# Performance work log

Hardware: AMD Instinct MI355X
Metric: run time of the kernel (lower is better)

## Reference

```python
import jax, jax.numpy as jnp
import numpy as np

P = 16                     # patch size
D = 192                    # embed dim (forced by SAT d_model=192)
NHEAD = 3                  # ViT-Tiny heads
SAT_H, SAT_DK, SAT_DV = 8, 32, 32
N_SLICE = 10
PER_LI = jnp.linspace(0.1, 1.0, N_SLICE)
LN_EPS = 1e-5


def layernorm(z, g, b):
    m = z.mean(-1, keepdims=True)
    v = ((z - m) ** 2).mean(-1, keepdims=True)
    return (z - m) * jax.lax.rsqrt(v + LN_EPS) * g + b


def setup_inputs() -> dict:
    key = jax.random.key(0)
    ks = jax.random.split(key, 32)
    B, IMG, DEPTH, MLP = 128, 224, 12, 4 * D
    S = (IMG // P) ** 2 + 1  # 197 tokens
    n = lambda k, sh: jax.random.normal(k, sh, jnp.float32) * 0.02
    z = lambda sh: jnp.zeros(sh, jnp.float32)
    o = lambda sh: jnp.ones(sh, jnp.float32)
    return {
        "x": jax.random.uniform(ks[0], (B, 3, IMG, IMG), jnp.float32),
        "x_g_norm": jax.random.uniform(ks[1], (B, 1, 56, 56), jnp.float32),
        "patch_w": n(ks[2], (D, 3, P, P)), "patch_b": z((D,)),
        "cls_token": n(ks[3], (1, 1, D)), "pos_embed": n(ks[4], (1, S, D)),
        "eleva_embed": n(ks[5], (1, D)),
        "sat_wq": n(ks[6], (D, SAT_H * SAT_DK)), "sat_bq": z((SAT_H * SAT_DK,)),
        "sat_wk": n(ks[7], (D, SAT_H * SAT_DK)), "sat_bk": z((SAT_H * SAT_DK,)),
        "sat_wv": n(ks[8], (D, SAT_H * SAT_DV)), "sat_bv": z((SAT_H * SAT_DV,)),
        "sat_wo": n(ks[9], (SAT_H * SAT_DV, D)), "sat_bo": z((D,)),
        "ln1_g": o((DEPTH, D)), "ln1_b": z((DEPTH, D)),
        "qkv_w": n(ks[10], (DEPTH, D, 3 * D)), "qkv_b": z((DEPTH, 3 * D)),
        "proj_w": n(ks[11], (DEPTH, D, D)), "proj_b": z((DEPTH, D)),
        "ln2_g": o((DEPTH, D)), "ln2_b": z((DEPTH, D)),
        "fc1_w": n(ks[12], (DEPTH, D, MLP)), "fc1_b": z((DEPTH, MLP)),
        "fc2_w": n(ks[13], (DEPTH, MLP, D)), "fc2_b": z((DEPTH, D)),
        "norm_g": o((D,)), "norm_b": z((D,)),
    }


def _forward(x, x_g_norm, patch_w, patch_b, cls_token, pos_embed, eleva_embed,
             sat_wq, sat_bq, sat_wk, sat_bk, sat_wv, sat_bv, sat_wo, sat_bo,
             ln1_g, ln1_b, qkv_w, qkv_b, proj_w, proj_b, ln2_g, ln2_b,
             fc1_w, fc1_b, fc2_w, fc2_b, norm_g, norm_b):
    B = x.shape[0]
    # --- patch embed: Conv2d(3, D, kernel=P, stride=P) -> [B, N, D] ---
    feat = jax.lax.conv_general_dilated(
        x, patch_w, (P, P), 'VALID', dimension_numbers=('NCHW', 'OIHW', 'NCHW'))
    feat = feat + patch_b[None, :, None, None]
    tokens = feat.reshape(B, D, -1).transpose(0, 2, 1)          # [B, 196, D]
    tok = jnp.concatenate([jnp.broadcast_to(cls_token, (B, 1, D)), tokens], axis=1)
    tok = tok + pos_embed                                        # [B, S, D]
    S = tok.shape[1]
    # --- elevation weight per sample (vectorized bisect + linear interp) ---
    means = x_g_norm.mean(axis=(1, 2, 3))                        # [B]
    idx = jnp.clip(jnp.searchsorted(PER_LI, means, side='left'), 0, N_SLICE - 1)
    per_hi = PER_LI[idx]
    per_lo = jnp.where(idx == 0, 0.0, PER_LI[jnp.maximum(idx - 1, 0)])
    idx_f = idx.astype(jnp.float32)
    idx_inter = idx_f - (per_hi - means) / (per_hi - per_lo)
    w = jnp.where(idx == N_SLICE - 1, idx_f, idx_inter) / N_SLICE  # [B]
    # --- SAT fusion: per (batch, token) a 2-element attention over (token, ele) ---
    ele = jnp.broadcast_to(eleva_embed[0] * w[:, None, None], tok.shape)  # [B,S,D]
    at_in = jnp.stack([tok, ele], axis=2)                        # [B, S, 2, D]
    q = (at_in @ sat_wq + sat_bq).reshape(B, S, 2, SAT_H, SAT_DK)
    k = (at_in @ sat_wk + sat_bk).reshape(B, S, 2, SAT_H, SAT_DK)
    v = (at_in @ sat_wv + sat_bv).reshape(B, S, 2, SAT_H, SAT_DV)
    att = jnp.einsum('bsqhd,bskhd->bshqk', q, k) * (1.0 / np.sqrt(SAT_DK))
    att = jax.nn.softmax(att, axis=-1)
    sat_o = jnp.einsum('bshqk,bskhd->bsqhd', att, v).reshape(B, S, 2, SAT_H * SAT_DV)
    sat_o = sat_o @ sat_wo + sat_bo                              # [B, S, 2, D]
    h = sat_o[..., 0, :] + sat_o[..., 1, :]                      # [B, S, D]
    # --- ViT blocks via scan over stacked layer params ---
    hd = D // NHEAD

    def block(z, p):
        l1g, l1b, qw, qb, pw, pb, l2g, l2b, f1w, f1b, f2w, f2b = p
        y = layernorm(z, l1g, l1b)
        qkv = y @ qw + qb                                        # [B, S, 3D]
        q_, k_, v_ = jnp.split(qkv, 3, axis=-1)
        q_ = q_.reshape(B, S, NHEAD, hd)
        k_ = k_.reshape(B, S, NHEAD, hd)
        v_ = v_.reshape(B, S, NHEAD, hd)
        a = jnp.einsum('bqhd,bkhd->bhqk', q_, k_) * (hd ** -0.5)
        a = jax.nn.softmax(a, axis=-1)
        o = jnp.einsum('bhqk,bkhd->bqhd', a, v_).reshape(B, S, D)
        z = z + o @ pw + pb
        y = layernorm(z, l2g, l2b)
        z = z + jax.nn.gelu(y @ f1w + f1b, approximate=False) @ f2w + f2b
        return z, None

    h, _ = jax.lax.scan(block, h, (ln1_g, ln1_b, qkv_w, qkv_b, proj_w, proj_b,
                                   ln2_g, ln2_b, fc1_w, fc1_b, fc2_w, fc2_b))
    h = layernorm(h, norm_g, norm_b)
    return h[:, 0]                                               # [B, D] cls token


def reference(x, x_g_norm, patch_w, patch_b, cls_token, pos_embed, eleva_embed,
              sat_wq, sat_bq, sat_wk, sat_bk, sat_wv, sat_bv, sat_wo, sat_bo,
              ln1_g, ln1_b, qkv_w, qkv_b, proj_w, proj_b, ln2_g, ln2_b,
              fc1_w, fc1_b, fc2_w, fc2_b, norm_g, norm_b):
    return _forward(x, x_g_norm, patch_w, patch_b, cls_token, pos_embed, eleva_embed,
                    sat_wq, sat_bq, sat_wk, sat_bk, sat_wv, sat_bv, sat_wo, sat_bo,
                    ln1_g, ln1_b, qkv_w, qkv_b, proj_w, proj_b, ln2_g, ln2_b,
                    fc1_w, fc1_b, fc2_w, fc2_b, norm_g, norm_b)
```

## Files before the change

### kernel.cpp

```cpp
#include <hip/hip_runtime.h>


#define BATCH 128
#define SEQ 197
#define BS_ROWS (BATCH * SEQ)
#define DMODEL 192
#define NPATCH 196
#define MROWS_PATCH (BATCH * NPATCH)
#define KPATCH 768
#define MLPDIM 768
#define DEPTH 12
#define SPAD 224

typedef float f32x4 __attribute__((ext_vector_type(4)));
typedef short s16x8 __attribute__((ext_vector_type(8)));

__device__ __forceinline__ float wredSum(float v) {
#pragma unroll
  for (int o = 32; o > 0; o >>= 1) v += __shfl_xor(v, o, 64);
  return v;
}

__device__ __forceinline__ unsigned short f2bf(float f) {
  union { float f; unsigned u; } v;
  v.f = f;
  unsigned r = v.u + 0x7FFFu + ((v.u >> 16) & 1u);
  return (unsigned short)(r >> 16);
}
__device__ __forceinline__ float bf2f(unsigned short u) {
  union { unsigned u; float f; } v;
  v.u = ((unsigned)u) << 16;
  return v.f;
}

__device__ __forceinline__ int swz(int col, int row) {
  int g8 = col >> 3;
  g8 = (g8 & ~7) | ((g8 & 7) ^ (row & 7));
  return (g8 << 3) | (col & 7);
}

__device__ __forceinline__ float gelu(float x) {
  const float ax = fabsf(x) * 0.70710678118654752f;
  const float t = 1.f / (1.f + 0.3275911f * ax);
  const float y =
      t * (0.254829592f +
           t * (-0.284496736f +
                t * (1.421413741f + t * (-1.453152027f + t * 1.061405429f))));
  const float erfc_ = y * __expf(-ax * ax);
  const float cdf = (x >= 0.f) ? (1.f - 0.5f * erfc_) : (0.5f * erfc_);
  return x * cdf;
}

__global__ __launch_bounds__(256) void eleva_w_kernel(const float* __restrict__ xg,
                                                      float* __restrict__ wout) {
  const int b = blockIdx.x;
  const float* p = xg + (size_t)b * 3136;
  float s = 0.f;
  for (int i = threadIdx.x; i < 3136; i += 256) s += p[i];
  __shared__ float partial[4];
  s = wredSum(s);
  if ((threadIdx.x & 63) == 0) partial[threadIdx.x >> 6] = s;
  __syncthreads();
  if (threadIdx.x == 0) {
    float m = (partial[0] + partial[1] + partial[2] + partial[3]) / 3136.f;
    int idx = 0;
#pragma unroll
    for (int i = 0; i < 10; i++) {
      float pv = 0.1f * (float)(i + 1);
      if (pv < m) idx = i + 1;
    }
    if (idx > 9) idx = 9;
    float wv;
    if (idx == 9) {
      wv = 9.f;
    } else {
      float hi = 0.1f * (float)(idx + 1);
      float lo = (idx == 0) ? 0.f : 0.1f * (float)idx;
      wv = (float)idx - (hi - m) / (hi - lo);
    }
    wout[b] = wv / 10.f;
  }
}

__global__ __launch_bounds__(256) void wtrans_kernel(const float* __restrict__ in,
                                                     unsigned short* __restrict__ out,
                                                     int R, int C) {
  const int z = blockIdx.z;
  in += (size_t)z * R * C;
  out += (size_t)z * R * C;
  const int c0 = blockIdx.x * 32, r0 = blockIdx.y * 32;
  __shared__ float t[32][33];
  const int tr = threadIdx.x >> 3, tc = (threadIdx.x & 7) * 4;
  const float4 v = *(const float4*)(in + (size_t)(r0 + tr) * C + c0 + tc);
  t[tr][tc] = v.x; t[tr][tc + 1] = v.y; t[tr][tc + 2] = v.z; t[tr][tc + 3] = v.w;
  __syncthreads();
  ushort4 o;
  o.x = f2bf(t[tc + 0][tr]);
  o.y = f2bf(t[tc + 1][tr]);
  o.z = f2bf(t[tc + 2][tr]);
  o.w = f2bf(t[tc + 3][tr]);
  const int brow = c0 + tr;
  *(ushort4*)(out + (size_t)brow * R + swz(r0 + tc, brow)) = o;
}

__global__ __launch_bounds__(256) void convert_kernel(const float* __restrict__ in,
                                                      unsigned short* __restrict__ out, int n4,
                                                      int K) {
  const int i = blockIdx.x * 256 + threadIdx.x;
  if (i >= n4) return;
  const int flat = i * 4;
  const int row = flat / K, col = flat % K;
  const float4 v = *(const float4*)(in + flat);
  ushort4 o;
  o.x = f2bf(v.x); o.y = f2bf(v.y); o.z = f2bf(v.z); o.w = f2bf(v.w);
  *(ushort4*)(out + (size_t)row * K + swz(col, row)) = o;
}

__global__ __launch_bounds__(256) void im2col_kernel(const float* __restrict__ x,
                                                     unsigned short* __restrict__ col) {
  const int i = blockIdx.x * 256 + threadIdx.x;
  if (i >= MROWS_PATCH * KPATCH / 8) return;
  const int k = (i % 96) * 8, row = i / 96;
  const int b = row / NPATCH, p = row % NPATCH;
  const int py = p / 14, px = p % 14;
  const int c = k >> 8, r = (k >> 4) & 15, cc = k & 15;
  const float* src = x + (((size_t)b * 3 + c) * 224 + (py * 16 + r)) * 224 + (px * 16 + cc);
  const float4 v0 = *(const float4*)src;
  const float4 v1 = *(const float4*)(src + 4);
  s16x8 o;
  o[0] = (short)f2bf(v0.x); o[1] = (short)f2bf(v0.y);
  o[2] = (short)f2bf(v0.z); o[3] = (short)f2bf(v0.w);
  o[4] = (short)f2bf(v1.x); o[5] = (short)f2bf(v1.y);
  o[6] = (short)f2bf(v1.z); o[7] = (short)f2bf(v1.w);
  *(s16x8*)(col + (size_t)row * KPATCH + swz(k, row)) = o;
}

__global__ __launch_bounds__(256) void cls_kernel(const float* __restrict__ cls,
                                                  const float* __restrict__ pos,
                                                  float* __restrict__ H,
                                                  unsigned short* __restrict__ Hbf) {
  const int i = blockIdx.x * 256 + threadIdx.x;
  if (i >= BATCH * DMODEL) return;
  const int b = i / DMODEL, d = i % DMODEL;
  const float v = cls[d] + pos[d];
  const int row = b * SEQ;
  H[(size_t)row * DMODEL + d] = v;
  Hbf[(size_t)row * DMODEL + swz(d, row)] = f2bf(v);
}

__global__ __launch_bounds__(256) void ele_proj_kernel(
    const float* __restrict__ ele_emb, const float* __restrict__ wq, const float* __restrict__ bq,
    const float* __restrict__ wk, const float* __restrict__ bk,
    const float* __restrict__ wv, const float* __restrict__ bv,
    const float* __restrict__ wvec, float* __restrict__ eq, float* __restrict__ ek,
    float* __restrict__ ev, float* __restrict__ satb) {
  const int b = blockIdx.x, t = threadIdx.x;
  if (b == 0) {
    satb[t] = bq[t];
    satb[256 + t] = bk[t];
    satb[512 + t] = bv[t];
  }
  __shared__ float es[DMODEL];
  if (t < DMODEL) es[t] = ele_emb[t] * wvec[b];
  __syncthreads();
  float aq = bq[t], ak = bk[t], av = bv[t];
  for (int d = 0; d < DMODEL; d++) {
    const float e = es[d];
    aq += e * wq[d * 256 + t];
    ak += e * wk[d * 256 + t];
    av += e * wv[d * 256 + t];
  }
  eq[b * 256 + t] = aq;
  ek[b * 256 + t] = ak;
  ev[b * 256 + t] = av;
}

__global__ __launch_bounds__(256) void sat_mix_kernel(
    const unsigned short* __restrict__ qkv768, const float* __restrict__ eq,
    const float* __restrict__ ek, const float* __restrict__ ev,
    unsigned short* __restrict__ o256) {
  const int gid = blockIdx.x * 256 + threadIdx.x;
  const int tok = gid >> 3, h = gid & 7;
  if (tok >= BS_ROWS) return;
  const int b = tok / SEQ;
  const unsigned short* qp = qkv768 + (size_t)tok * 768 + h * 32;
  s16x8 qv[4], kv[4];
#pragma unroll
  for (int i0 = 0; i0 < 4; i0++) {
    qv[i0] = *(const s16x8*)(qp + i0 * 8);
    kv[i0] = *(const s16x8*)(qp + 256 + i0 * 8);
  }
  float eqa[32], eka[32];
  {
    const float4* eqp = (const float4*)(eq + b * 256 + h * 32);
    const float4* ekp = (const float4*)(ek + b * 256 + h * 32);
#pragma unroll
    for (int i0 = 0; i0 < 8; i0++) {
      const float4 a = eqp[i0], c = ekp[i0];
      eqa[i0 * 4] = a.x; eqa[i0 * 4 + 1] = a.y; eqa[i0 * 4 + 2] = a.z; eqa[i0 * 4 + 3] = a.w;
      eka[i0 * 4] = c.x; eka[i0 * 4 + 1] = c.y; eka[i0 * 4 + 2] = c.z; eka[i0 * 4 + 3] = c.w;
    }
  }
  float s00 = 0.f, s01 = 0.f, s10 = 0.f, s11 = 0.f;
#pragma unroll
  for (int d = 0; d < 32; d++) {
    const float q_ = bf2f((unsigned short)qv[d >> 3][d & 7]);
    const float k_ = bf2f((unsigned short)kv[d >> 3][d & 7]);
    s00 += q_ * k_;
    s01 += q_ * eka[d];
    s10 += eqa[d] * k_;
    s11 += eqa[d] * eka[d];
  }
  const float sc = 0.17677669529663687f;
  s00 *= sc; s01 *= sc; s10 *= sc; s11 *= sc;
  const float m0 = fmaxf(s00, s01), m1 = fmaxf(s10, s11);
  const float e00 = __expf(s00 - m0), e01 = __expf(s01 - m0);
  const float e10 = __expf(s10 - m1), e11 = __expf(s11 - m1);
  const float w0 = e00 / (e00 + e01) + e10 / (e10 + e11);
  const float w1 = e01 / (e00 + e01) + e11 / (e10 + e11);
  unsigned short* op = o256 + (size_t)tok * 256;
  const float4* evp = (const float4*)(ev + b * 256 + h * 32);
#pragma unroll
  for (int i0 = 0; i0 < 4; i0++) {
    const s16x8 vv = *(const s16x8*)(qp + 512 + i0 * 8);
    const float4 e0 = evp[i0 * 2], e1 = evp[i0 * 2 + 1];
    float ev8[8] = {e0.x, e0.y, e0.z, e0.w, e1.x, e1.y, e1.z, e1.w};
    s16x8 o;
#pragma unroll
    for (int e = 0; e < 8; e++)
      o[e] = (short)f2bf(w0 * bf2f((unsigned short)vv[e]) + w1 * ev8[e]);
    *(s16x8*)(op + swz(h * 32 + i0 * 8, tok)) = o;
  }
}

template <int EPI, bool SWZO, int BN>
__global__ __launch_bounds__(256, (BN == 96) ? 4 : 1)
void gemm_mfma(const unsigned short* __restrict__ A,
               const unsigned short* __restrict__ Bt,
               const float* __restrict__ bias,
               const float* __restrict__ res,
               void* __restrict__ Cout,
               unsigned short* __restrict__ aux_hbf,
               const float* __restrict__ aux_pos,
               const float* __restrict__ lng,
               const float* __restrict__ lnb,
               int M, int N, int K) {
  constexpr int NJ = BN / 32;
  constexpr bool LNF = (EPI == 5 || EPI == 6);
  __shared__ unsigned short As[128 * 64];
  __shared__ unsigned short Bs[BN * 64];
  __shared__ float2 lnbuf[2][128];
  const int tid = threadIdx.x, lane = tid & 63, w = tid >> 6;
  const int n0 = blockIdx.x * BN;
  const int m0 = blockIdx.y * 128;
  const int c = lane & 15, g = lane >> 4;
  const int wm = (w >> 1) * 64, wn = (w & 1) * (BN / 2);
  f32x4 acc[4][NJ] = {};

  const int ar = (lane >> 3);
  const int acol = (lane & 7) * 8;

  for (int k0 = 0; k0 < K; k0 += 64) {
#pragma unroll
    for (int it = 0; it < 4; it++) {
      const int r = w * 32 + it * 8 + ar;
      const unsigned short* gp = A + (size_t)(m0 + r) * K + k0 + acol;
      __builtin_amdgcn_global_load_lds(
          (const __attribute__((address_space(1))) unsigned int*)gp,
          (__attribute__((address_space(3))) unsigned int*)(As + w * 2048 + it * 512),
          16, 0, 0);
    }
#pragma unroll
    for (int it = 0; it < NJ; it++) {
      const int r = w * (BN / 4) + it * 8 + ar;
      const unsigned short* gp = Bt + (size_t)(n0 + r) * K + k0 + acol;
      __builtin_amdgcn_global_load_lds(
          (const __attribute__((address_space(1))) unsigned int*)gp,
          (__attribute__((address_space(3))) unsigned int*)(Bs + (w * (BN / 4) + it * 8) * 64),
          16, 0, 0);
    }
    __syncthreads();
#pragma unroll
    for (int kk = 0; kk < 2; kk++) {
      const int sw = (((kk * 4 + g) ^ (c & 7))) << 3;
      s16x8 af[4], bfr[NJ];
#pragma unroll
      for (int i = 0; i < 4; i++)
        af[i] = *(const s16x8*)&As[(wm + i * 16 + c) * 64 + sw];
#pragma unroll
      for (int j = 0; j < NJ; j++)
        bfr[j] = *(const s16x8*)&Bs[(wn + j * 16 + c) * 64 + sw];
#pragma unroll
      for (int i = 0; i < 4; i++)
#pragma unroll
        for (int j = 0; j < NJ; j++)
          acc[i][j] = __builtin_amdgcn_mfma_f32_16x16x32_bf16(af[i], bfr[j], acc[i][j], 0, 0, 0);
    }
    __syncthreads();
  }

  const int ncol0 = n0 + wn + c;
  float bv[NJ];
#pragma unroll
  for (int j = 0; j < NJ; j++) bv[j] = bias[ncol0 + j * 16] * (EPI == 6 ? 2.f : 1.f);

  if constexpr (LNF) {
    const int p = w & 1;
#pragma unroll
    for (int i = 0; i < 4; i++) {
#pragma unroll
      for (int r_ = 0; r_ < 4; r_++) {
        const int lr = wm + i * 16 + g * 4 + r_;
        const int mrow = m0 + lr;
        float s1 = 0.f, s2 = 0.f;
#pragma unroll
        for (int j = 0; j < NJ; j++) {
          float v = acc[i][j][r_] + bv[j];
          if (EPI == 5) v += res[(size_t)mrow * DMODEL + ncol0 + j * 16];
          acc[i][j][r_] = v;
          ((float*)Cout)[(size_t)mrow * DMODEL + ncol0 + j * 16] = v;
          s1 += v;
          s2 += v * v;
        }
#pragma unroll
        for (int o = 1; o <= 8; o <<= 1) {
          s1 += __shfl_xor(s1, o, 64);
          s2 += __shfl_xor(s2, o, 64);
        }
        if (c == 0) lnbuf[p][lr] = make_float2(s1, s2);
      }
    }
    __syncthreads();
    float lg[NJ], lb[NJ];
#pragma unroll
    for (int j = 0; j < NJ; j++) { lg[j] = lng[ncol0 + j * 16]; lb[j] = lnb[ncol0 + j * 16]; }
#pragma unroll
    for (int i = 0; i < 4; i++) {
#pragma unroll
      for (int r_ = 0; r_ < 4; r_++) {
        const int lr = wm + i * 16 + g * 4 + r_;
        const int mrow = m0 + lr;
        const float2 a0 = lnbuf[0][lr], a1 = lnbuf[1][lr];
        const float mean = (a0.x + a1.x) * (1.f / 192.f);
        const float var = (a0.y + a1.y) * (1.f / 192.f) - mean * mean;
        const float inv = rsqrtf(var + 1e-5f);
#pragma unroll
        for (int j = 0; j < NJ; j++) {
          const int col = ncol0 + j * 16;
          const float yn = (acc[i][j][r_] - mean) * inv * lg[j] + lb[j];
          aux_hbf[(size_t)mrow * DMODEL + swz(col, mrow)] = f2bf(yn);
        }
      }
    }
  } else {
#pragma unroll
    for (int i = 0; i < 4; i++) {
#pragma unroll
      for (int r_ = 0; r_ < 4; r_++) {
        const int mrow = m0 + wm + i * 16 + g * 4 + r_;
        if (EPI == 4) {
          const int bb = mrow / 196;
          const int p = mrow - bb * 196;
          const int drow = mrow + bb + 1;
#pragma unroll
          for (int j = 0; j < NJ; j++) {
            const int col = ncol0 + j * 16;
            const float v = acc[i][j][r_] + bv[j] + aux_pos[(size_t)(p + 1) * DMODEL + col];
            ((float*)Cout)[(size_t)drow * DMODEL + col] = v;
            aux_hbf[(size_t)drow * DMODEL + swz(col, drow)] = f2bf(v);
          }
        } else {
#pragma unroll
          for (int j = 0; j < NJ; j++) {
            float v = acc[i][j][r_] + bv[j];
            const int col = ncol0 + j * 16;
            const size_t rowoff = (size_t)mrow * N;
            if (EPI == 0) {
              ((unsigned short*)Cout)[rowoff + (SWZO ? swz(col, mrow) : col)] = f2bf(v);
            } else {
              ((unsigned short*)Cout)[rowoff + (SWZO ? swz(col, mrow) : col)] = f2bf(gelu(v));
            }
          }
        }
      }
    }
  }
}

__global__ __launch_bounds__(256) void final_ln_kernel(const float* __restrict__ H,
                                                       const float* __restrict__ g,
                                                       const float* __restrict__ bta,
                                                       float* __restrict__ out) {
  const int w = threadIdx.x >> 6, lane = threadIdx.x & 63;
  const int bi = blockIdx.x * 4 + w;
  if (bi >= BATCH) return;
  const float* x = H + (size_t)bi * SEQ * DMODEL;
  const float x0 = x[lane], x1 = x[lane + 64], x2 = x[lane + 128];
  const float m = wredSum(x0 + x1 + x2) * (1.f / 192.f);
  const float d0 = x0 - m, d1 = x1 - m, d2 = x2 - m;
  const float v = wredSum(d0 * d0 + d1 * d1 + d2 * d2) * (1.f / 192.f);
  const float inv = rsqrtf(v + 1e-5f);
  float* y = out + (size_t)bi * DMODEL;
  y[lane] = d0 * inv * g[lane] + bta[lane];
  y[lane + 64] = d1 * inv * g[lane + 64] + bta[lane + 64];
  y[lane + 128] = d2 * inv * g[lane + 128] + bta[lane + 128];
}

__global__ __launch_bounds__(256) void vtrans_kernel(const unsigned short* __restrict__ qkv,
                                                     unsigned short* __restrict__ vt) {
  const int bid = blockIdx.x;
  const int sc = bid & 3, bh = bid >> 2;
  const int b = bh / 3, h = bh % 3;
  const int s0 = sc * 64;
  __shared__ unsigned short t[64][72];
  const int tid = threadIdx.x;
  for (int e = tid; e < 64 * 64; e += 256) {
    const int sp = e >> 6, d = e & 63;
    const int s = s0 + sp;
    t[sp][d] = (s < SEQ) ? qkv[((size_t)(b * SEQ + s)) * 576 + 384 + h * 64 + d] : (unsigned short)0;
  }
  __syncthreads();
  for (int e = tid; e < 64 * 64; e += 256) {
    const int d = e >> 6, sp = e & 63;
    const int s = s0 + sp;
    if (s < SPAD) vt[((size_t)bh * 64 + d) * SPAD + s] = t[sp][d];
  }
}

__global__ __launch_bounds__(64) void attn_mfma_kernel(const unsigned short* __restrict__ qkv,
                                                       const unsigned short* __restrict__ vt,
                                                       unsigned short* __restrict__ out) {
  const int bid = blockIdx.x;
  const int bh = bid / 13, qt = bid % 13;
  const int b = bh / 3, h = bh % 3;
  const int row0 = b * SEQ;
  const int q0 = qt * 16;
  const int lane = threadIdx.x;
  const int c = lane & 15, g = lane >> 4;

  __shared__ __attribute__((aligned(16))) unsigned short P[16][232];

  const int qr = row0 + min(q0 + c, SEQ - 1);
  const unsigned short* qp = qkv + (size_t)qr * 576 + h * 64 + g * 8;
  const s16x8 qlo = *(const s16x8*)qp;
  const s16x8 qhi = *(const s16x8*)(qp + 32);

  f32x4 acc[13];
#pragma unroll
  for (int t = 0; t < 13; t++) {
    const int kr = row0 + min(t * 16 + c, SEQ - 1);
    const unsigned short* kp = qkv + (size_t)kr * 576 + 192 + h * 64 + g * 8;
    const s16x8 klo = *(const s16x8*)kp;
    const s16x8 khi = *(const s16x8*)(kp + 32);
    f32x4 z = {0.f, 0.f, 0.f, 0.f};
    z = __builtin_amdgcn_mfma_f32_16x16x32_bf16(qlo, klo, z, 0, 0, 0);
    acc[t] = __builtin_amdgcn_mfma_f32_16x16x32_bf16(qhi, khi, z, 0, 0, 0);
  }

  const bool m12 = (c >= 5);
#pragma unroll
  for (int r = 0; r < 4; r++) {
    float mx = -INFINITY;
#pragma unroll
    for (int t = 0; t < 13; t++) {
      const float v = (t == 12 && m12) ? -INFINITY : acc[t][r];
      mx = fmaxf(mx, v);
    }
#pragma unroll
    for (int o = 1; o <= 8; o <<= 1) mx = fmaxf(mx, __shfl_xor(mx, o, 64));
    const float ms = mx * 0.125f;
    float sum = 0.f;
#pragma unroll
    for (int t = 0; t < 13; t++) {
      const float e = (t == 12 && m12) ? 0.f : __expf(acc[t][r] * 0.125f - ms);
      acc[t][r] = e;
      sum += e;
    }
#pragma unroll
    for (int o = 1; o <= 8; o <<= 1) sum += __shfl_xor(sum, o, 64);
    const float inv = 1.f / sum;
#pragma unroll
    for (int t = 0; t < 13; t++) P[g * 4 + r][t * 16 + c] = f2bf(acc[t][r] * inv);
  }
  {
    unsigned short z4[4] = {0, 0, 0, 0};
    *(uint2*)&P[c][208 + g * 4] = *(uint2*)z4;
  }
  __builtin_amdgcn_s_waitcnt(0);

  f32x4 oacc[4];
#pragma unroll
  for (int dt = 0; dt < 4; dt++) oacc[dt] = (f32x4){0.f, 0.f, 0.f, 0.f};
  const unsigned short* vbase = vt + (size_t)bh * 64 * SPAD;
#pragma unroll
  for (int ch = 0; ch < 7; ch++) {
    const s16x8 pa = *(const s16x8*)&P[c][ch * 32 + g * 8];
#pragma unroll
    for (int dt = 0; dt < 4; dt++) {
      const s16x8 vb = *(const s16x8*)(vbase + (size_t)(dt * 16 + c) * SPAD + ch * 32 + g * 8);
      oacc[dt] = __builtin_amdgcn_mfma_f32_16x16x32_bf16(pa, vb, oacc[dt], 0, 0, 0);
    }
  }

#pragma unroll
  for (int dt = 0; dt < 4; dt++) {
#pragma unroll
    for (int r = 0; r < 4; r++) {
      const int q = q0 + g * 4 + r;
      if (q < SEQ) {
        const int trow = row0 + q;
        out[(size_t)trow * DMODEL + swz(h * 64 + dt * 16 + c, trow)] = f2bf(oacc[dt][r]);
      }
    }
  }
}

extern "C" void kernel_launch(void* const* d_in, const int* in_sizes, int n_in,
                              void* d_out, int out_size, void* d_ws, size_t ws_size,
                              hipStream_t stream) {
  const float* x       = (const float*)d_in[0];
  const float* xg      = (const float*)d_in[1];
  const float* patch_w = (const float*)d_in[2];
  const float* patch_b = (const float*)d_in[3];
  const float* cls_tok = (const float*)d_in[4];
  const float* pos_emb = (const float*)d_in[5];
  const float* ele_emb = (const float*)d_in[6];
  const float* sat_wq  = (const float*)d_in[7];
  const float* sat_bq  = (const float*)d_in[8];
  const float* sat_wk  = (const float*)d_in[9];
  const float* sat_bk  = (const float*)d_in[10];
  const float* sat_wv  = (const float*)d_in[11];
  const float* sat_bv  = (const float*)d_in[12];
  const float* sat_wo  = (const float*)d_in[13];
  const float* sat_bo  = (const float*)d_in[14];
  const float* ln1_g   = (const float*)d_in[15];
  const float* ln1_b   = (const float*)d_in[16];
  const float* qkv_w   = (const float*)d_in[17];
  const float* qkv_b   = (const float*)d_in[18];
  const float* proj_w  = (const float*)d_in[19];
  const float* proj_b  = (const float*)d_in[20];
  const float* ln2_g   = (const float*)d_in[21];
  const float* ln2_b   = (const float*)d_in[22];
  const float* fc1_w   = (const float*)d_in[23];
  const float* fc1_b   = (const float*)d_in[24];
  const float* fc2_w   = (const float*)d_in[25];
  const float* fc2_b   = (const float*)d_in[26];
  const float* norm_g  = (const float*)d_in[27];
  const float* norm_b  = (const float*)d_in[28];
  float* out = (float*)d_out;
  float* ws = (float*)d_ws;

  float* W_ELE = ws;
  float* EQ = ws + 256;
  float* EK = EQ + 32768;
  float* EV = EK + 32768;
  float* H = ws + 98560;
  unsigned short* Hbf   = (unsigned short*)(ws + 4940032);
  unsigned short* Ybf   = (unsigned short*)(ws + 7360768);
  unsigned short* QKVbf = (unsigned short*)(ws + 9781504);
  unsigned short* MLPbf = (unsigned short*)(ws + 17043712);
  unsigned short* VTB   = (unsigned short*)(ws + 26726656);
  unsigned short* WTS   = (unsigned short*)(ws + 29479168);
  float* SATB = ws + 32305408;
  unsigned short* ATTNbf = (unsigned short*)(ws + 32306176);

  unsigned short* qkv_wt   = WTS;
  unsigned short* proj_wt  = WTS + 1327104;
  unsigned short* fc1_wt   = WTS + 1769472;
  unsigned short* fc2_wt   = WTS + 3538944;
  unsigned short* patch_bf = WTS + 5308416;
  unsigned short* satqkv_t = WTS + 5455872;
  unsigned short* sato_t   = WTS + 5603328;

  unsigned short* COLbf   = MLPbf;
  unsigned short* SATQKV  = MLPbf;
  unsigned short* O256bf  = QKVbf;

  wtrans_kernel<<<dim3(18, 6, 12), 256, 0, stream>>>(qkv_w, qkv_wt, 192, 576);
  wtrans_kernel<<<dim3(6, 6, 12), 256, 0, stream>>>(proj_w, proj_wt, 192, 192);
  wtrans_kernel<<<dim3(24, 6, 12), 256, 0, stream>>>(fc1_w, fc1_wt, 192, 768);
  wtrans_kernel<<<dim3(6, 24, 12), 256, 0, stream>>>(fc2_w, fc2_wt, 768, 192);
  wtrans_kernel<<<dim3(8, 6, 1), 256, 0, stream>>>(sat_wq, satqkv_t, 192, 256);
  wtrans_kernel<<<dim3(8, 6, 1), 256, 0, stream>>>(sat_wk, satqkv_t + 49152, 192, 256);
  wtrans_kernel<<<dim3(8, 6, 1), 256, 0, stream>>>(sat_wv, satqkv_t + 98304, 192, 256);
  wtrans_kernel<<<dim3(6, 8, 1), 256, 0, stream>>>(sat_wo, sato_t, 256, 192);
  convert_kernel<<<144, 256, 0, stream>>>(patch_w, patch_bf, 36864, KPATCH);

  eleva_w_kernel<<<BATCH, 256, 0, stream>>>(xg, W_ELE);

  im2col_kernel<<<(MROWS_PATCH * KPATCH / 8) / 256, 256, 0, stream>>>(x, COLbf);
  gemm_mfma<4, false, 96><<<dim3(2, 196), 256, 0, stream>>>(
      COLbf, patch_bf, patch_b, nullptr, H, Hbf, pos_emb, nullptr, nullptr,
      MROWS_PATCH, DMODEL, KPATCH);
  cls_kernel<<<(BATCH * DMODEL) / 256, 256, 0, stream>>>(cls_tok, pos_emb, H, Hbf);

  ele_proj_kernel<<<BATCH, 256, 0, stream>>>(ele_emb, sat_wq, sat_bq, sat_wk, sat_bk,
                                             sat_wv, sat_bv, W_ELE, EQ, EK, EV, SATB);
  gemm_mfma<0, false, 96><<<dim3(8, 197), 256, 0, stream>>>(
      Hbf, satqkv_t, SATB, nullptr, SATQKV, nullptr, nullptr, nullptr, nullptr,
      BS_ROWS, 768, DMODEL);
  sat_mix_kernel<<<BS_ROWS / 32, 256, 0, stream>>>(SATQKV, EQ, EK, EV, O256bf);
  gemm_mfma<6, false, 192><<<dim3(1, 197), 256, 0, stream>>>(
      O256bf, sato_t, sat_bo, nullptr, H, Ybf, nullptr, ln1_g, ln1_b,
      BS_ROWS, DMODEL, 256);

  for (int l = 0; l < DEPTH; l++) {
    gemm_mfma<0, false, 96><<<dim3(6, 197), 256, 0, stream>>>(
        Ybf, qkv_wt + (size_t)l * 110592, qkv_b + l * 576, nullptr, QKVbf, nullptr, nullptr,
        nullptr, nullptr, BS_ROWS, 576, DMODEL);
    vtrans_kernel<<<BATCH * 3 * 4, 256, 0, stream>>>(QKVbf, VTB);
    attn_mfma_kernel<<<BATCH * 3 * 13, 64, 0, stream>>>(QKVbf, VTB, ATTNbf);
    gemm_mfma<5, false, 192><<<dim3(1, 197), 256, 0, stream>>>(
        ATTNbf, proj_wt + (size_t)l * 36864, proj_b + l * DMODEL, H, H, Ybf, nullptr,
        ln2_g + l * DMODEL, ln2_b + l * DMODEL, BS_ROWS, DMODEL, DMODEL);
    gemm_mfma<1, true, 96><<<dim3(8, 197), 256, 0, stream>>>(
        Ybf, fc1_wt + (size_t)l * 147456, fc1_b + l * MLPDIM, nullptr, MLPbf, nullptr, nullptr,
        nullptr, nullptr, BS_ROWS, MLPDIM, DMODEL);
    const float* nlg = (l < DEPTH - 1) ? (ln1_g + (l + 1) * DMODEL) : norm_g;
    const float* nlb = (l < DEPTH - 1) ? (ln1_b + (l + 1) * DMODEL) : norm_b;
    gemm_mfma<5, false, 192><<<dim3(1, 197), 256, 0, stream>>>(
        MLPbf, fc2_wt + (size_t)l * 147456, fc2_b + l * DMODEL, H, H, Ybf, nullptr,
        nlg, nlb, BS_ROWS, DMODEL, MLPDIM);
  }

  final_ln_kernel<<<BATCH / 4, 256, 0, stream>>>(H, norm_g, norm_b, out);
}
```

Measured before the change: 1.890 ms.

## Use 32-row tiles with 4-wave column split for LayerNorm-fused GEMMs

Adds a BM template parameter to the MFMA GEMM. The N=192 GEMMs with fused LayerNorm epilogue (proj, fc2, SAT output) now use 32-row tiles, with each of the four waves owning 48 columns, launched on 788 blocks instead of 197. The LN partial sums are reduced across four waves through shared memory. This is meant to fix the poor occupancy and low block count of the old 128x192 tile, which ran at one block per CU and left much of the GPU idle. The cost is less reuse of the B tile per block and more weight reloads from global memory.

```diff
diff --git a/kernel.cpp b/kernel.cpp
--- a/kernel.cpp
+++ b/kernel.cpp
@@ -233,8 +233,8 @@
   }
 }
 
-template <int EPI, bool SWZO, int BN>
-__global__ __launch_bounds__(256, (BN == 96) ? 4 : 1)
+template <int EPI, bool SWZO, int BN, int BM>
+__global__ __launch_bounds__(256, 4)
 void gemm_mfma(const unsigned short* __restrict__ A,
                const unsigned short* __restrict__ Bt,
                const float* __restrict__ bias,
@@ -245,33 +245,36 @@
                const float* __restrict__ lng,
                const float* __restrict__ lnb,
                int M, int N, int K) {
-  constexpr int NJ = BN / 32;
+  constexpr int NJ = 3;
+  constexpr int MI = (BM == 128) ? 4 : 2;
   constexpr bool LNF = (EPI == 5 || EPI == 6);
-  __shared__ unsigned short As[128 * 64];
+  constexpr int LNROWS = LNF ? BM : 1;
+  __shared__ unsigned short As[BM * 64];
   __shared__ unsigned short Bs[BN * 64];
-  __shared__ float2 lnbuf[2][128];
+  __shared__ float2 lnbuf[4][LNROWS];
   const int tid = threadIdx.x, lane = tid & 63, w = tid >> 6;
   const int n0 = blockIdx.x * BN;
-  const int m0 = blockIdx.y * 128;
+  const int m0 = blockIdx.y * BM;
   const int c = lane & 15, g = lane >> 4;
-  const int wm = (w >> 1) * 64, wn = (w & 1) * (BN / 2);
-  f32x4 acc[4][NJ] = {};
+  const int wm = (BM == 128) ? (w >> 1) * 64 : 0;
+  const int wn = (BM == 128) ? (w & 1) * 96 / 2 : w * 48;
+  f32x4 acc[MI][NJ] = {};
 
   const int ar = (lane >> 3);
   const int acol = (lane & 7) * 8;
 
   for (int k0 = 0; k0 < K; k0 += 64) {
 #pragma unroll
-    for (int it = 0; it < 4; it++) {
-      const int r = w * 32 + it * 8 + ar;
+    for (int it = 0; it < BM / 32; it++) {
+      const int r = w * (BM / 4) + it * 8 + ar;
       const unsigned short* gp = A + (size_t)(m0 + r) * K + k0 + acol;
       __builtin_amdgcn_global_load_lds(
           (const __attribute__((address_space(1))) unsigned int*)gp,
-          (__attribute__((address_space(3))) unsigned int*)(As + w * 2048 + it * 512),
+          (__attribute__((address_space(3))) unsigned int*)(As + (w * (BM / 4) + it * 8) * 64),
           16, 0, 0);
     }
 #pragma unroll
-    for (int it = 0; it < NJ; it++) {
+    for (int it = 0; it < BN / 32; it++) {
       const int r = w * (BN / 4) + it * 8 + ar;
       const unsigned short* gp = Bt + (size_t)(n0 + r) * K + k0 + acol;
       __builtin_amdgcn_global_load_lds(
@@ -283,15 +286,15 @@
 #pragma unroll
     for (int kk = 0; kk < 2; kk++) {
       const int sw = (((kk * 4 + g) ^ (c & 7))) << 3;
-      s16x8 af[4], bfr[NJ];
-#pragma unroll
-      for (int i = 0; i < 4; i++)
+      s16x8 af[MI], bfr[NJ];
+#pragma unroll
+      for (int i = 0; i < MI; i++)
         af[i] = *(const s16x8*)&As[(wm + i * 16 + c) * 64 + sw];
 #pragma unroll
       for (int j = 0; j < NJ; j++)
         bfr[j] = *(const s16x8*)&Bs[(wn + j * 16 + c) * 64 + sw];
 #pragma unroll
-      for (int i = 0; i < 4; i++)
+      for (int i = 0; i < MI; i++)
 #pragma unroll
         for (int j = 0; j < NJ; j++)
           acc[i][j] = __builtin_amdgcn_mfma_f32_16x16x32_bf16(af[i], bfr[j], acc[i][j], 0, 0, 0);
@@ -305,9 +308,8 @@
   for (int j = 0; j < NJ; j++) bv[j] = bias[ncol0 + j * 16] * (EPI == 6 ? 2.f : 1.f);
 
   if constexpr (LNF) {
-    const int p = w & 1;
-#pragma unroll
-    for (int i = 0; i < 4; i++) {
+#pragma unroll
+    for (int i = 0; i < MI; i++) {
 #pragma unroll
       for (int r_ = 0; r_ < 4; r_++) {
         const int lr = wm + i * 16 + g * 4 + r_;
@@ -327,7 +329,7 @@
           s1 += __shfl_xor(s1, o, 64);
           s2 += __shfl_xor(s2, o, 64);
         }
-        if (c == 0) lnbuf[p][lr] = make_float2(s1, s2);
+        if (c == 0) lnbuf[w][lr] = make_float2(s1, s2);
       }
     }
     __syncthreads();
@@ -335,14 +337,15 @@
 #pragma unroll
     for (int j = 0; j < NJ; j++) { lg[j] = lng[ncol0 + j * 16]; lb[j] = lnb[ncol0 + j * 16]; }
 #pragma unroll
-    for (int i = 0; i < 4; i++) {
+    for (int i = 0; i < MI; i++) {
 #pragma unroll
       for (int r_ = 0; r_ < 4; r_++) {
         const int lr = wm + i * 16 + g * 4 + r_;
         const int mrow = m0 + lr;
         const float2 a0 = lnbuf[0][lr], a1 = lnbuf[1][lr];
-        const float mean = (a0.x + a1.x) * (1.f / 192.f);
-        const float var = (a0.y + a1.y) * (1.f / 192.f) - mean * mean;
+        const float2 a2 = lnbuf[2][lr], a3 = lnbuf[3][lr];
+        const float mean = (a0.x + a1.x + a2.x + a3.x) * (1.f / 192.f);
+        const float var = (a0.y + a1.y + a2.y + a3.y) * (1.f / 192.f) - mean * mean;
         const float inv = rsqrtf(var + 1e-5f);
 #pragma unroll
         for (int j = 0; j < NJ; j++) {
@@ -354,7 +357,7 @@
     }
   } else {
 #pragma unroll
-    for (int i = 0; i < 4; i++) {
+    for (int i = 0; i < MI; i++) {
 #pragma unroll
       for (int r_ = 0; r_ < 4; r_++) {
         const int mrow = m0 + wm + i * 16 + g * 4 + r_;
@@ -589,36 +592,36 @@
   eleva_w_kernel<<<BATCH, 256, 0, stream>>>(xg, W_ELE);
 
   im2col_kernel<<<(MROWS_PATCH * KPATCH / 8) / 256, 256, 0, stream>>>(x, COLbf);
-  gemm_mfma<4, false, 96><<<dim3(2, 196), 256, 0, stream>>>(
+  gemm_mfma<4, false, 96, 128><<<dim3(2, 196), 256, 0, stream>>>(
       COLbf, patch_bf, patch_b, nullptr, H, Hbf, pos_emb, nullptr, nullptr,
       MROWS_PATCH, DMODEL, KPATCH);
   cls_kernel<<<(BATCH * DMODEL) / 256, 256, 0, stream>>>(cls_tok, pos_emb, H, Hbf);
 
   ele_proj_kernel<<<BATCH, 256, 0, stream>>>(ele_emb, sat_wq, sat_bq, sat_wk, sat_bk,
                                              sat_wv, sat_bv, W_ELE, EQ, EK, EV, SATB);
-  gemm_mfma<0, false, 96><<<dim3(8, 197), 256, 0, stream>>>(
+  gemm_mfma<0, false, 96, 128><<<dim3(8, 197), 256, 0, stream>>>(
       Hbf, satqkv_t, SATB, nullptr, SATQKV, nullptr, nullptr, nullptr, nullptr,
       BS_ROWS, 768, DMODEL);
   sat_mix_kernel<<<BS_ROWS / 32, 256, 0, stream>>>(SATQKV, EQ, EK, EV, O256bf);
-  gemm_mfma<6, false, 192><<<dim3(1, 197), 256, 0, stream>>>(
+  gemm_mfma<6, false, 192, 32><<<dim3(1, 788), 256, 0, stream>>>(
       O256bf, sato_t, sat_bo, nullptr, H, Ybf, nullptr, ln1_g, ln1_b,
       BS_ROWS, DMODEL, 256);
 
   for (int l = 0; l < DEPTH; l++) {
-    gemm_mfma<0, false, 96><<<dim3(6, 197), 256, 0, stream>>>(
+    gemm_mfma<0, false, 96, 128><<<dim3(6, 197), 256, 0, stream>>>(
         Ybf, qkv_wt + (size_t)l * 110592, qkv_b + l * 576, nullptr, QKVbf, nullptr, nullptr,
         nullptr, nullptr, BS_ROWS, 576, DMODEL);
     vtrans_kernel<<<BATCH * 3 * 4, 256, 0, stream>>>(QKVbf, VTB);
     attn_mfma_kernel<<<BATCH * 3 * 13, 64, 0, stream>>>(QKVbf, VTB, ATTNbf);
-    gemm_mfma<5, false, 192><<<dim3(1, 197), 256, 0, stream>>>(
+    gemm_mfma<5, false, 192, 32><<<dim3(1, 788), 256, 0, stream>>>(
         ATTNbf, proj_wt + (size_t)l * 36864, proj_b + l * DMODEL, H, H, Ybf, nullptr,
         ln2_g + l * DMODEL, ln2_b + l * DMODEL, BS_ROWS, DMODEL, DMODEL);
-    gemm_mfma<1, true, 96><<<dim3(8, 197), 256, 0, stream>>>(
+    gemm_mfma<1, true, 96, 128><<<dim3(8, 197), 256, 0, stream>>>(
         Ybf, fc1_wt + (size_t)l * 147456, fc1_b + l * MLPDIM, nullptr, MLPbf, nullptr, nullptr,
         nullptr, nullptr, BS_ROWS, MLPDIM, DMODEL);
     const float* nlg = (l < DEPTH - 1) ? (ln1_g + (l + 1) * DMODEL) : norm_g;
     const float* nlb = (l < DEPTH - 1) ? (ln1_b + (l + 1) * DMODEL) : norm_b;
-    gemm_mfma<5, false, 192><<<dim3(1, 197), 256, 0, stream>>>(
+    gemm_mfma<5, false, 192, 32><<<dim3(1, 788), 256, 0, stream>>>(
         MLPbf, fc2_wt + (size_t)l * 147456, fc2_b + l * DMODEL, H, H, Ybf, nullptr,
         nlg, nlb, BS_ROWS, DMODEL, MLPDIM);
   }
```

After: 1.759 ms. 6.9% less time.
